# Kernel tuning notes

Hardware: AMD Instinct MI355X
Metric: run time of the kernel (lower is better)

## Reference

```python
import jax, jax.numpy as jnp
import numpy as np

B, N, C, HEADS = 8, 1024, 768, 12
HW = 32  # H = W = 32, so H*W == N


def _layernorm(x, g, b, eps=1e-5):
    mu = x.mean(-1, keepdims=True)
    var = ((x - mu) ** 2).mean(-1, keepdims=True)
    return (x - mu) * jax.lax.rsqrt(var + eps) * g + b


def setup_inputs() -> dict:
    key = jax.random.key(0)
    ks = jax.random.split(key, 6)
    w = lambda k, shape: jax.random.normal(k, shape, dtype=jnp.float32) * 0.02
    return {
        "x": jax.random.normal(ks[0], (B, N, C), dtype=jnp.float32),
        "y": jax.random.normal(ks[1], (B, C, HW, HW), dtype=jnp.float32),
        "q_w": w(ks[2], (C, C)),
        "q_b": jnp.zeros((C,), jnp.float32),
        "kv_w": w(ks[3], (2 * C, C)),
        "kv_b": jnp.zeros((2 * C,), jnp.float32),
        "proj_w": w(ks[4], (C, C)),
        "proj_b": jnp.zeros((C,), jnp.float32),
        "ln_g": jnp.ones((C,), jnp.float32),
        "ln_b": jnp.zeros((C,), jnp.float32),
        "H": HW,
        "W": HW,
    }


def reference(x, y, q_w, q_b, kv_w, kv_b, proj_w, proj_b, ln_g, ln_b, H, W):
    Bn, Nn, Cn = x.shape
    hd = Cn // HEADS
    scale = hd ** -0.5  # qk_scale=None, c_ratio=1 -> head_dim**-0.5

    # gating tensors from y
    y1 = y.reshape(Bn, Cn, H * W).transpose(0, 2, 1)          # [B, N, C]
    y2 = _layernorm(y1, ln_g, ln_b)
    yq = jax.nn.sigmoid(y2 @ q_w.T + q_b)                      # [B, N, C]
    ykv = jax.nn.sigmoid(y2 @ kv_w.T + kv_b)                   # [B, N, 2C]

    # gated q: q2 = q0 + q0*yq
    q0 = x @ q_w.T + q_b
    q = (q0 + q0 * yq).reshape(Bn, Nn, HEADS, hd).transpose(0, 2, 1, 3)  # [B,h,N,d]

    # gated kv: kv2 = kv0*ykv + ykv
    kv0 = x @ kv_w.T + kv_b
    kv = (kv0 * ykv + ykv).reshape(Bn, Nn, 2, HEADS, hd).transpose(2, 0, 3, 1, 4)
    k, v = kv[0], kv[1]                                        # [B,h,N,d] each

    attn = jax.nn.softmax(jnp.einsum("bhqd,bhkd->bhqk", q, k) * scale, axis=-1)
    out = jnp.einsum("bhqk,bhkd->bhqd", attn, v)
    out = out.transpose(0, 2, 1, 3).reshape(Bn, Nn, Cn)
    return out @ proj_w.T + proj_b
```

## Files before the change

kernel.cpp:

```cpp
#include <hip/hip_runtime.h>
#include <stdint.h>

typedef __attribute__((ext_vector_type(4))) float f4;
typedef __attribute__((ext_vector_type(8))) short bf16x8;
typedef __attribute__((ext_vector_type(4))) unsigned short u16x4;
typedef unsigned short u16;

#define B_ 8
#define N_ 1024
#define C_ 768
#define NH 12
#define HD 64

__device__ __forceinline__ float bf2f(u16 v) {
  union { unsigned u; float f; } x; x.u = ((unsigned)v) << 16; return x.f;
}
__device__ __forceinline__ u16 f2bf(float f) {
  union { float f; unsigned u; } x; x.f = f;
  unsigned r = x.u + 0x7FFFu + ((x.u >> 16) & 1u);
  return (u16)(r >> 16);
}
__device__ __forceinline__ void g2l16(const u16* g, const u16* l) {
  __builtin_amdgcn_global_load_lds(
      (const __attribute__((address_space(1))) void*)(uintptr_t)g,
      (__attribute__((address_space(3))) void*)(uint32_t)(uintptr_t)l,
      16, 0, 0);
}

#define SW6() asm volatile("s_waitcnt vmcnt(6)" ::: "memory")
#define SW4() asm volatile("s_waitcnt vmcnt(4)" ::: "memory")
#define SW3() asm volatile("s_waitcnt vmcnt(3)" ::: "memory")
#define SW0() asm volatile("s_waitcnt vmcnt(0)" ::: "memory")
#define BARF()                              \
  do {                                      \
    __builtin_amdgcn_s_barrier();           \
    asm volatile("" ::: "memory");          \
    __builtin_amdgcn_sched_barrier(0);      \
  } while (0)

__global__ __launch_bounds__(256) void cvt_bf16(const float* __restrict__ s,
                                                u16* __restrict__ d, int n4) {
  int i = blockIdx.x * 256 + threadIdx.x;
  int stride = gridDim.x * 256;
  for (; i < n4; i += stride) {
    float4 v = ((const float4*)s)[i];
    u16x4 o;
    o.x = f2bf(v.x); o.y = f2bf(v.y); o.z = f2bf(v.z); o.w = f2bf(v.w);
    ((u16x4*)d)[i] = o;
  }
}

__global__ __launch_bounds__(256) void ln_stats(const float* __restrict__ y,
                                                float* __restrict__ mu,
                                                float* __restrict__ rs,
                                                int b0) {
  __shared__ float s1[4][64], s2[4][64];
  int t = threadIdx.x;
  int nl = t & 63, ch = t >> 6;
  int idx0 = b0 * N_ + blockIdx.x * 64;
  int b = idx0 >> 10, nb_ = idx0 & 1023;
  const float* p = y + (size_t)b * C_ * N_ + nb_ + nl;
  float s = 0.f, q = 0.f;
  int c0 = ch * 192;
  for (int c = c0; c < c0 + 192; ++c) {
    float v = p[(size_t)c * N_];
    s += v; q += v * v;
  }
  s1[ch][nl] = s; s2[ch][nl] = q;
  __syncthreads();
  if (t < 64) {
    float ts = s1[0][t] + s1[1][t] + s1[2][t] + s1[3][t];
    float tq = s2[0][t] + s2[1][t] + s2[2][t] + s2[3][t];
    float m = ts * (1.f / C_);
    float var = tq * (1.f / C_) - m * m;
    mu[idx0 + t] = m;
    rs[idx0 + t] = rsqrtf(fmaxf(var, 0.f) + 1e-5f);
  }
}

__global__ __launch_bounds__(256) void ln_apply(const float* __restrict__ y,
                                                const float* __restrict__ mu,
                                                const float* __restrict__ rs,
                                                const float* __restrict__ lg,
                                                const float* __restrict__ lb,
                                                u16* __restrict__ y2c,
                                                int b0) {
  __shared__ float tile[64][65];
  int t = threadIdx.x;
  int n0 = blockIdx.x * 64, c0 = blockIdx.y * 64;
  int bl = blockIdx.z, b = b0 + bl;
  int jc = (t & 15) * 4, ir = t >> 4;
  for (int r = 0; r < 4; ++r) {
    int i = ir + r * 16;
    float4 v = *(const float4*)(y + ((size_t)b * C_ + c0 + i) * N_ + n0 + jc);
    tile[i][jc] = v.x; tile[i][jc + 1] = v.y; tile[i][jc + 2] = v.z; tile[i][jc + 3] = v.w;
  }
  __syncthreads();
  for (int r = 0; r < 4; ++r) {
    int i = ir + r * 16;
    int n = n0 + i;
    float m = mu[b * N_ + n], rr = rs[b * N_ + n];
    float g0 = lg[c0 + jc],     b0f = lb[c0 + jc];
    float g1 = lg[c0 + jc + 1], b1f = lb[c0 + jc + 1];
    float g2 = lg[c0 + jc + 2], b2f = lb[c0 + jc + 2];
    float g3 = lg[c0 + jc + 3], b3f = lb[c0 + jc + 3];
    u16x4 o;
    o.x = f2bf((tile[jc][i] - m) * rr * g0 + b0f);
    o.y = f2bf((tile[jc + 1][i] - m) * rr * g1 + b1f);
    o.z = f2bf((tile[jc + 2][i] - m) * rr * g2 + b2f);
    o.w = f2bf((tile[jc + 3][i] - m) * rr * g3 + b3f);
    *(u16x4*)(y2c + ((size_t)bl * N_ + n) * C_ + c0 + jc) = o;
  }
}

__global__ __launch_bounds__(256, 2) void gemm_gate(
    const u16* __restrict__ xbc, const u16* __restrict__ y2c,
    const u16* __restrict__ qwb, const u16* __restrict__ kvwb,
    const float* __restrict__ qb_, const float* __restrict__ kvb_,
    u16* __restrict__ o_q, u16* __restrict__ o_k, u16* __restrict__ o_vT) {
  __shared__ u16 smem[24576];
  int t = threadIdx.x, l = t & 63;
  int quad = l >> 4, l15 = l & 15;
  int w = t >> 6, wm = w & 1, wn = w >> 1;
  int m0l = blockIdx.x * 128;
  int n0l = blockIdx.y * 128;

  const u16* wp; const float* bp; int sel, h0;
  if (n0l < C_) {
    wp = qwb + (size_t)n0l * C_; bp = qb_ + n0l; sel = 0; h0 = n0l >> 6;
  } else {
    int nk = n0l - C_;
    wp = kvwb + (size_t)nk * C_; bp = kvb_ + nk;
    sel = (nk < C_) ? 1 : 2;
    h0 = ((sel == 2) ? nk - C_ : nk) >> 6;
  }

  f4 accx[4][4], accy[4][4];
  for (int i = 0; i < 4; ++i)
    for (int j = 0; j < 4; ++j) {
      accx[i][j] = (f4){0.f, 0.f, 0.f, 0.f};
      accy[i][j] = (f4){0.f, 0.f, 0.f, 0.f};
    }

  int row = t >> 2, colb = (t & 3) * 8;
  const u16* gx = xbc + (size_t)(m0l + row) * C_ + colb;
  const u16* gy = y2c + (size_t)(m0l + row) * C_ + colb;
  const u16* gw = wp + (size_t)row * C_ + colb;

#define STAGE_G(OFF, kk)                                   \
  do {                                                     \
    u16* p_ = smem + (OFF);                                \
    g2l16(gx + (kk),           p_ + t * 8);                \
    g2l16(gx + (kk) + 64 * C_, p_ + 2048 + t * 8);         \
    g2l16(gy + (kk),           p_ + 4096 + t * 8);         \
    g2l16(gy + (kk) + 64 * C_, p_ + 6144 + t * 8);         \
    g2l16(gw + (kk),           p_ + 8192 + t * 8);         \
    g2l16(gw + (kk) + 64 * C_, p_ + 10240 + t * 8);        \
  } while (0)

#define COMPUTE_G(OFF)                                                        \
  do {                                                                        \
    const u16* base = smem + (OFF);                                           \
    bf16x8 afx[4], afy[4], bfr[4];                                            \
    for (int i = 0; i < 4; ++i) {                                             \
      int ra = (wm * 64 + i * 16 + l15) * 32 + quad * 8;                      \
      afx[i] = *(const bf16x8*)&base[ra];                                     \
      afy[i] = *(const bf16x8*)&base[4096 + ra];                              \
      int rb = (wn * 64 + i * 16 + l15) * 32 + quad * 8;                      \
      bfr[i] = *(const bf16x8*)&base[8192 + rb];                              \
    }                                                                         \
    for (int i = 0; i < 4; ++i)                                               \
      for (int j = 0; j < 4; ++j) {                                           \
        accx[i][j] = __builtin_amdgcn_mfma_f32_16x16x32_bf16(afx[i], bfr[j], accx[i][j], 0, 0, 0); \
        accy[i][j] = __builtin_amdgcn_mfma_f32_16x16x32_bf16(afy[i], bfr[j], accy[i][j], 0, 0, 0); \
      }                                                                       \
  } while (0)

  STAGE_G(0, 0);
  STAGE_G(12288, 32);
  SW6();
  BARF();
  for (int n = 0; n < 24; n += 2) {
    COMPUTE_G(0);
    BARF();
    if (n + 2 < 24) { STAGE_G(0, (n + 2) * 32); SW6(); } else { SW0(); }
    BARF();
    COMPUTE_G(12288);
    BARF();
    if (n + 3 < 24) { STAGE_G(12288, (n + 3) * 32); SW6(); } else { SW0(); }
    BARF();
  }
#undef STAGE_G
#undef COMPUTE_G

  const int PITCH = 136;
  for (int j = 0; j < 4; ++j) {
    int cloc = wn * 64 + j * 16 + l15;
    float bias = bp[cloc];
    for (int i = 0; i < 4; ++i) {
      int rb0 = wm * 64 + i * 16 + quad * 4;
      for (int r = 0; r < 4; ++r) {
        int rloc = rb0 + r;
        float vx = accx[i][j][r] + bias;
        float vy = accy[i][j][r] + bias;
        float gg = 1.f / (1.f + __expf(-vy));
        float val = (sel == 0) ? vx * (1.f + gg) : gg * (vx + 1.f);
        u16 bv = f2bf(val);
        if (sel == 2) smem[cloc * PITCH + rloc] = bv;
        else          smem[rloc * PITCH + cloc] = bv;
      }
    }
  }
  __syncthreads();
  {
    int rr = t >> 1, hh = t & 1;
    const u16* src = smem + rr * PITCH + hh * 64;
    u16* dst;
    if (sel == 2) {
      int h = h0 + (rr >> 6), d = rr & 63;
      int bl = m0l >> 10, nbase = m0l & 1023;
      dst = o_vT + (size_t)((bl * NH + h) * HD + d) * N_ + nbase + hh * 64;
    } else {
      int gml = m0l + rr;
      int bl = gml >> 10, n = gml & 1023;
      int h = h0 + hh;
      dst = (sel == 0 ? o_q : o_k) + (size_t)((bl * NH + h) * N_ + n) * HD;
    }
    for (int c = 0; c < 8; ++c) {
      bf16x8 v = *(const bf16x8*)(src + c * 8);
      *(bf16x8*)(dst + c * 8) = v;
    }
  }
}

__global__ __launch_bounds__(256) void attn(const u16* __restrict__ qoc,
                                            const u16* __restrict__ koc,
                                            const u16* __restrict__ vTc,
                                            u16* __restrict__ aoc) {
  __shared__ u16 Qs[4096], Ks[8192], Vs[8192];
  __shared__ u16 Ps[64 * 72];
  int t = threadIdx.x, l = t & 63, w = t >> 6;
  int quad = l >> 4, l15 = l & 15;
  int bhl = blockIdx.y;
  int bl = bhl / NH, h = bhl % NH;
  int q0 = blockIdx.x * 64;
  int sr = t >> 3;
  int swo = ((t & 7) ^ (sr & 7)) * 8;
  const u16* qbp = qoc + ((size_t)bhl * N_ + q0) * HD;
  const u16* kb = koc + (size_t)bhl * N_ * HD;
  const u16* vb = vTc + (size_t)bhl * HD * N_;

#define STAGE_KV(OFF, key0)                                                   \
  do {                                                                        \
    g2l16(kb + (size_t)((key0) + sr) * HD + swo,      Ks + (OFF) + t * 8);    \
    g2l16(kb + (size_t)((key0) + 32 + sr) * HD + swo, Ks + (OFF) + 2048 + t * 8); \
    g2l16(vb + (size_t)sr * N_ + (key0) + swo,        Vs + (OFF) + t * 8);    \
    g2l16(vb + (size_t)(32 + sr) * N_ + (key0) + swo, Vs + (OFF) + 2048 + t * 8); \
  } while (0)

  g2l16(qbp + sr * HD + swo,        Qs + t * 8);
  g2l16(qbp + (32 + sr) * HD + swo, Qs + 2048 + t * 8);
  STAGE_KV(0, 0);
  STAGE_KV(4096, 64);
  SW4();
  BARF();

  int sA = (quad ^ (l15 & 7)) * 8;
  int sB = sA ^ 32;
  bf16x8 aq0 = *(const bf16x8*)&Qs[(w * 16 + l15) * 64 + sA];
  bf16x8 aq1 = *(const bf16x8*)&Qs[(w * 16 + l15) * 64 + sB];
  f4 o[4];
  for (int i = 0; i < 4; ++i) o[i] = (f4){0.f, 0.f, 0.f, 0.f};
  f4 ls = (f4){0.f, 0.f, 0.f, 0.f};
  bf16x8 ones;
  for (int i = 0; i < 8; ++i) ones[i] = (short)0x3F80;

#define TILE_STEP(KOFF)                                                       \
  do {                                                                        \
    f4 s_[4];                                                                 \
    __builtin_amdgcn_s_setprio(1);                                            \
    for (int ni = 0; ni < 4; ++ni) {                                          \
      bf16x8 b0v = *(const bf16x8*)&Ks[(KOFF) + (ni * 16 + l15) * 64 + sA];   \
      bf16x8 b1v = *(const bf16x8*)&Ks[(KOFF) + (ni * 16 + l15) * 64 + sB];   \
      f4 z = (f4){0.f, 0.f, 0.f, 0.f};                                        \
      z = __builtin_amdgcn_mfma_f32_16x16x32_bf16(aq0, b0v, z, 0, 0, 0);      \
      z = __builtin_amdgcn_mfma_f32_16x16x32_bf16(aq1, b1v, z, 0, 0, 0);      \
      s_[ni] = z;                                                             \
    }                                                                         \
    __builtin_amdgcn_s_setprio(0);                                            \
    for (int ni = 0; ni < 4; ++ni)                                            \
      for (int r = 0; r < 4; ++r)                                             \
        Ps[(w * 16 + quad * 4 + r) * 72 + ni * 16 + l15] =                    \
            f2bf(__expf(s_[ni][r] * 0.125f));                                 \
    bf16x8 ap0 = *(const bf16x8*)&Ps[(w * 16 + l15) * 72 + quad * 8];         \
    bf16x8 ap1 = *(const bf16x8*)&Ps[(w * 16 + l15) * 72 + 32 + quad * 8];    \
    __builtin_amdgcn_s_setprio(1);                                            \
    for (int ni = 0; ni < 4; ++ni) {                                          \
      bf16x8 b0v = *(const bf16x8*)&Vs[(KOFF) + (ni * 16 + l15) * 64 + sA];   \
      bf16x8 b1v = *(const bf16x8*)&Vs[(KOFF) + (ni * 16 + l15) * 64 + sB];   \
      o[ni] = __builtin_amdgcn_mfma_f32_16x16x32_bf16(ap0, b0v, o[ni], 0, 0, 0); \
      o[ni] = __builtin_amdgcn_mfma_f32_16x16x32_bf16(ap1, b1v, o[ni], 0, 0, 0); \
    }                                                                         \
    ls = __builtin_amdgcn_mfma_f32_16x16x32_bf16(ap0, ones, ls, 0, 0, 0);     \
    ls = __builtin_amdgcn_mfma_f32_16x16x32_bf16(ap1, ones, ls, 0, 0, 0);     \
    __builtin_amdgcn_s_setprio(0);                                            \
  } while (0)

  for (int kt = 0; kt < 16; kt += 2) {
    TILE_STEP(0);
    BARF();
    if (kt + 2 < 16) { STAGE_KV(0, (kt + 2) * 64); SW4(); } else { SW0(); }
    BARF();
    TILE_STEP(4096);
    BARF();
    if (kt + 3 < 16) { STAGE_KV(4096, (kt + 3) * 64); SW4(); } else { SW0(); }
    BARF();
  }
#undef TILE_STEP
#undef STAGE_KV

  for (int ni = 0; ni < 4; ++ni)
    for (int r = 0; r < 4; ++r)
      Ps[(w * 16 + quad * 4 + r) * 72 + ni * 16 + l15] =
          f2bf(o[ni][r] / ls[r]);
  __syncthreads();
  {
    int rr = t >> 2, cc = t & 3;
    int n = q0 + rr;
    const u16* src = Ps + rr * 72 + cc * 16;
    u16* dst = aoc + ((size_t)bl * N_ + n) * C_ + h * HD + cc * 16;
    *(bf16x8*)dst = *(const bf16x8*)src;
    *(bf16x8*)(dst + 8) = *(const bf16x8*)(src + 8);
  }
}

__global__ __launch_bounds__(256, 2) void gemm_proj(const u16* __restrict__ aoc,
                                                    const u16* __restrict__ pwb,
                                                    const float* __restrict__ bias,
                                                    float* __restrict__ out,
                                                    int b0) {
  __shared__ u16 smem[12288];
  int t = threadIdx.x, l = t & 63;
  int quad = l >> 4, l15 = l & 15;
  int w = t >> 6, wm = w & 1, wn = w >> 1;
  int m0l = blockIdx.x * 128, n0 = blockIdx.y * 64;
  f4 acc[4][2];
  for (int i = 0; i < 4; ++i)
    for (int j = 0; j < 2; ++j) acc[i][j] = (f4){0.f, 0.f, 0.f, 0.f};
  int row = t >> 2, colb = (t & 3) * 8;
  const u16* ga = aoc + (size_t)(m0l + row) * C_ + colb;
  const u16* gw = pwb + (size_t)(n0 + row) * C_ + colb;

#define STAGE_P(OFF, kk)                                   \
  do {                                                     \
    u16* p_ = smem + (OFF);                                \
    g2l16(ga + (kk),           p_ + t * 8);                \
    g2l16(ga + (kk) + 64 * C_, p_ + 2048 + t * 8);         \
    g2l16(gw + (kk),           p_ + 4096 + t * 8);         \
  } while (0)

#define COMPUTE_P(OFF)                                                        \
  do {                                                                        \
    const u16* base = smem + (OFF);                                           \
    bf16x8 af[4], bfr[2];                                                     \
    for (int i = 0; i < 4; ++i)                                               \
      af[i] = *(const bf16x8*)&base[(wm * 64 + i * 16 + l15) * 32 + quad * 8];\
    for (int j = 0; j < 2; ++j)                                               \
      bfr[j] = *(const bf16x8*)&base[4096 + (wn * 32 + j * 16 + l15) * 32 + quad * 8]; \
    for (int i = 0; i < 4; ++i)                                               \
      for (int j = 0; j < 2; ++j)                                             \
        acc[i][j] = __builtin_amdgcn_mfma_f32_16x16x32_bf16(af[i], bfr[j], acc[i][j], 0, 0, 0); \
  } while (0)

  STAGE_P(0, 0);
  STAGE_P(6144, 32);
  SW3();
  BARF();
  for (int n = 0; n < 24; n += 2) {
    COMPUTE_P(0);
    BARF();
    if (n + 2 < 24) { STAGE_P(0, (n + 2) * 32); SW3(); } else { SW0(); }
    BARF();
    COMPUTE_P(6144);
    BARF();
    if (n + 3 < 24) { STAGE_P(6144, (n + 3) * 32); SW3(); } else { SW0(); }
    BARF();
  }
#undef STAGE_P
#undef COMPUTE_P

  for (int j = 0; j < 2; ++j) {
    int gcol = n0 + wn * 32 + j * 16 + l15;
    float bv = bias[gcol];
    for (int i = 0; i < 4; ++i) {
      int rbase = m0l + wm * 64 + i * 16 + quad * 4;
      for (int r = 0; r < 4; ++r)
        __builtin_nontemporal_store(acc[i][j][r] + bv,
                                    &out[(size_t)(b0 * N_ + rbase + r) * C_ + gcol]);
    }
  }
}

extern "C" void kernel_launch(void* const* d_in, const int* in_sizes, int n_in,
                              void* d_out, int out_size, void* d_ws, size_t ws_size,
                              hipStream_t stream) {
  const float* x   = (const float*)d_in[0];
  const float* y   = (const float*)d_in[1];
  const float* qw  = (const float*)d_in[2];
  const float* qb  = (const float*)d_in[3];
  const float* kvw = (const float*)d_in[4];
  const float* kvb = (const float*)d_in[5];
  const float* pw  = (const float*)d_in[6];
  const float* pb  = (const float*)d_in[7];
  const float* lg  = (const float*)d_in[8];
  const float* lb  = (const float*)d_in[9];

  char* ws = (char*)d_ws;
  float* mu = (float*)(ws);
  float* rs = (float*)(ws + 32768);
  u16* qwb  = (u16*)(ws + 65536);
  u16* kvwb = (u16*)(ws + 1245184);
  u16* pwb  = (u16*)(ws + 3604480);
  const size_t BASE2 = 4784128;
  const size_t PER_B = 1572864;

  int nb = 1;
  for (int c = 8; c >= 1; c >>= 1) {
    if (BASE2 + 5 * (size_t)c * PER_B <= ws_size) { nb = c; break; }
  }
  u16* xbc = (u16*)(ws + BASE2);
  u16* y2c = (u16*)(ws + BASE2 + (size_t)nb * PER_B);
  u16* qoc = (u16*)(ws + BASE2 + 2 * (size_t)nb * PER_B);
  u16* koc = (u16*)(ws + BASE2 + 3 * (size_t)nb * PER_B);
  u16* vTc = (u16*)(ws + BASE2 + 4 * (size_t)nb * PER_B);
  u16* aoc = xbc;

  cvt_bf16<<<dim3(576), dim3(256), 0, stream>>>(qw, qwb, 147456);
  cvt_bf16<<<dim3(1152), dim3(256), 0, stream>>>(kvw, kvwb, 294912);
  cvt_bf16<<<dim3(576), dim3(256), 0, stream>>>(pw, pwb, 147456);

  for (int b0 = 0; b0 < B_; b0 += nb) {
    cvt_bf16<<<dim3(768 * nb), dim3(256), 0, stream>>>(
        x + (size_t)b0 * N_ * C_, xbc, nb * 196608);
    ln_stats<<<dim3(16 * nb), dim3(256), 0, stream>>>(y, mu, rs, b0);
    ln_apply<<<dim3(16, 12, nb), dim3(256), 0, stream>>>(y, mu, rs, lg, lb, y2c, b0);
    gemm_gate<<<dim3(8 * nb, 18), dim3(256), 0, stream>>>(xbc, y2c, qwb, kvwb,
                                                          qb, kvb, qoc, koc, vTc);
    attn<<<dim3(16, 12 * nb), dim3(256), 0, stream>>>(qoc, koc, vTc, aoc);
    gemm_proj<<<dim3(8 * nb, 12), dim3(256), 0, stream>>>(aoc, pwb, pb, (float*)d_out, b0);
  }
}
```

Measured before the change: 281.5 us.

## Triple-buffer GEMM LDS pipelines and XOR-swizzle tiles to avoid bank conflicts

Both the gated QKV GEMM and the projection GEMM move from double- to triple-buffered LDS staging, keeping two tile loads in flight while computing on a third. The global-to-LDS copy addresses and the MFMA fragment reads get an XOR swizzle on the 8-element column chunk, meant to cut LDS bank conflicts on the 32-wide rows. The loops, including the attention kernel's tile loop, are fully unrolled. The extra LDS (72KB for gemm_gate) may reduce occupancy below the two blocks per CU the launch bounds request.

Measured after the change: 285.3 us. No clear change (+1.4%).

```diff
diff --git a/kernel.cpp b/kernel.cpp
--- a/kernel.cpp
+++ b/kernel.cpp
@@ -27,10 +27,11 @@
       16, 0, 0);
 }
 
-#define SW6() asm volatile("s_waitcnt vmcnt(6)" ::: "memory")
-#define SW4() asm volatile("s_waitcnt vmcnt(4)" ::: "memory")
-#define SW3() asm volatile("s_waitcnt vmcnt(3)" ::: "memory")
-#define SW0() asm volatile("s_waitcnt vmcnt(0)" ::: "memory")
+#define SW12() asm volatile("s_waitcnt vmcnt(12)" ::: "memory")
+#define SW6()  asm volatile("s_waitcnt vmcnt(6)" ::: "memory")
+#define SW4()  asm volatile("s_waitcnt vmcnt(4)" ::: "memory")
+#define SW3()  asm volatile("s_waitcnt vmcnt(3)" ::: "memory")
+#define SW0()  asm volatile("s_waitcnt vmcnt(0)" ::: "memory")
 #define BARF()                              \
   do {                                      \
     __builtin_amdgcn_s_barrier();           \
@@ -118,7 +119,7 @@
     const u16* __restrict__ qwb, const u16* __restrict__ kvwb,
     const float* __restrict__ qb_, const float* __restrict__ kvb_,
     u16* __restrict__ o_q, u16* __restrict__ o_k, u16* __restrict__ o_vT) {
-  __shared__ u16 smem[24576];
+  __shared__ u16 smem[36864];
   int t = threadIdx.x, l = t & 63;
   int quad = l >> 4, l15 = l & 15;
   int w = t >> 6, wm = w & 1, wn = w >> 1;
@@ -142,10 +143,12 @@
       accy[i][j] = (f4){0.f, 0.f, 0.f, 0.f};
     }
 
-  int row = t >> 2, colb = (t & 3) * 8;
-  const u16* gx = xbc + (size_t)(m0l + row) * C_ + colb;
-  const u16* gy = y2c + (size_t)(m0l + row) * C_ + colb;
-  const u16* gw = wp + (size_t)row * C_ + colb;
+  int row = t >> 2;
+  int colS = (((t & 3) ^ (row & 3)) * 8);
+  const u16* gx = xbc + (size_t)(m0l + row) * C_ + colS;
+  const u16* gy = y2c + (size_t)(m0l + row) * C_ + colS;
+  const u16* gw = wp + (size_t)row * C_ + colS;
+  int rsl = (quad ^ (l15 & 3)) * 8;
 
 #define STAGE_G(OFF, kk)                                   \
   do {                                                     \
@@ -163,10 +166,10 @@
     const u16* base = smem + (OFF);                                           \
     bf16x8 afx[4], afy[4], bfr[4];                                            \
     for (int i = 0; i < 4; ++i) {                                             \
-      int ra = (wm * 64 + i * 16 + l15) * 32 + quad * 8;                      \
+      int ra = (wm * 64 + i * 16 + l15) * 32 + rsl;                           \
       afx[i] = *(const bf16x8*)&base[ra];                                     \
       afy[i] = *(const bf16x8*)&base[4096 + ra];                              \
-      int rb = (wn * 64 + i * 16 + l15) * 32 + quad * 8;                      \
+      int rb = (wn * 64 + i * 16 + l15) * 32 + rsl;                           \
       bfr[i] = *(const bf16x8*)&base[8192 + rb];                              \
     }                                                                         \
     for (int i = 0; i < 4; ++i)                                               \
@@ -176,20 +179,28 @@
       }                                                                       \
   } while (0)
 
+#define STEP_G(i, OFF)                                        \
+  do {                                                        \
+    COMPUTE_G(OFF);                                           \
+    BARF();                                                   \
+    if ((i) < 21)      { STAGE_G(OFF, ((i) + 3) * 32); SW12(); } \
+    else if ((i) == 21) SW6();                                \
+    else if ((i) == 22) SW0();                                \
+    BARF();                                                   \
+  } while (0)
+
   STAGE_G(0, 0);
   STAGE_G(12288, 32);
-  SW6();
+  STAGE_G(24576, 64);
+  SW12();
   BARF();
-  for (int n = 0; n < 24; n += 2) {
-    COMPUTE_G(0);
-    BARF();
-    if (n + 2 < 24) { STAGE_G(0, (n + 2) * 32); SW6(); } else { SW0(); }
-    BARF();
-    COMPUTE_G(12288);
-    BARF();
-    if (n + 3 < 24) { STAGE_G(12288, (n + 3) * 32); SW6(); } else { SW0(); }
-    BARF();
-  }
+#pragma unroll
+  for (int n = 0; n < 24; n += 3) {
+    STEP_G(n, 0);
+    STEP_G(n + 1, 12288);
+    STEP_G(n + 2, 24576);
+  }
+#undef STEP_G
 #undef STAGE_G
 #undef COMPUTE_G
 
@@ -306,6 +317,7 @@
     __builtin_amdgcn_s_setprio(0);                                            \
   } while (0)
 
+#pragma unroll
   for (int kt = 0; kt < 16; kt += 2) {
     TILE_STEP(0);
     BARF();
@@ -339,7 +351,7 @@
                                                     const float* __restrict__ bias,
                                                     float* __restrict__ out,
                                                     int b0) {
-  __shared__ u16 smem[12288];
+  __shared__ u16 smem[18432];
   int t = threadIdx.x, l = t & 63;
   int quad = l >> 4, l15 = l & 15;
   int w = t >> 6, wm = w & 1, wn = w >> 1;
@@ -347,9 +359,11 @@
   f4 acc[4][2];
   for (int i = 0; i < 4; ++i)
     for (int j = 0; j < 2; ++j) acc[i][j] = (f4){0.f, 0.f, 0.f, 0.f};
-  int row = t >> 2, colb = (t & 3) * 8;
-  const u16* ga = aoc + (size_t)(m0l + row) * C_ + colb;
-  const u16* gw = pwb + (size_t)(n0 + row) * C_ + colb;
+  int row = t >> 2;
+  int colS = (((t & 3) ^ (row & 3)) * 8);
+  const u16* ga = aoc + (size_t)(m0l + row) * C_ + colS;
+  const u16* gw = pwb + (size_t)(n0 + row) * C_ + colS;
+  int rsl = (quad ^ (l15 & 3)) * 8;
 
 #define STAGE_P(OFF, kk)                                   \
   do {                                                     \
@@ -364,28 +378,36 @@
     const u16* base = smem + (OFF);                                           \
     bf16x8 af[4], bfr[2];                                                     \
     for (int i = 0; i < 4; ++i)                                               \
-      af[i] = *(const bf16x8*)&base[(wm * 64 + i * 16 + l15) * 32 + quad * 8];\
+      af[i] = *(const bf16x8*)&base[(wm * 64 + i * 16 + l15) * 32 + rsl];     \
     for (int j = 0; j < 2; ++j)                                               \
-      bfr[j] = *(const bf16x8*)&base[4096 + (wn * 32 + j * 16 + l15) * 32 + quad * 8]; \
+      bfr[j] = *(const bf16x8*)&base[4096 + (wn * 32 + j * 16 + l15) * 32 + rsl]; \
     for (int i = 0; i < 4; ++i)                                               \
       for (int j = 0; j < 2; ++j)                                             \
         acc[i][j] = __builtin_amdgcn_mfma_f32_16x16x32_bf16(af[i], bfr[j], acc[i][j], 0, 0, 0); \
   } while (0)
 
+#define STEP_P(i, OFF)                                        \
+  do {                                                        \
+    COMPUTE_P(OFF);                                           \
+    BARF();                                                   \
+    if ((i) < 21)      { STAGE_P(OFF, ((i) + 3) * 32); SW6(); } \
+    else if ((i) == 21) SW3();                                \
+    else if ((i) == 22) SW0();                                \
+    BARF();                                                   \
+  } while (0)
+
   STAGE_P(0, 0);
   STAGE_P(6144, 32);
-  SW3();
+  STAGE_P(12288, 64);
+  SW6();
   BARF();
-  for (int n = 0; n < 24; n += 2) {
-    COMPUTE_P(0);
-    BARF();
-    if (n + 2 < 24) { STAGE_P(0, (n + 2) * 32); SW3(); } else { SW0(); }
-    BARF();
-    COMPUTE_P(6144);
-    BARF();
-    if (n + 3 < 24) { STAGE_P(6144, (n + 3) * 32); SW3(); } else { SW0(); }
-    BARF();
-  }
+#pragma unroll
+  for (int n = 0; n < 24; n += 3) {
+    STEP_P(n, 0);
+    STEP_P(n + 1, 6144);
+    STEP_P(n + 2, 12288);
+  }
+#undef STEP_P
 #undef STAGE_P
 #undef COMPUTE_P
 
```
